# Kernel tuning notes

Measured on AMD Instinct MI355X. Metric: run time of the kernel, lower is better.

## Reference

```python
import jax, jax.numpy as jnp
import numpy as np

HEAD_SIZE = 64


def setup_inputs() -> dict:
    key = jax.random.key(0)
    ks = jax.random.split(key, 6)
    B, S, D, H = 8, 2048, 1024, HEAD_SIZE
    return {
        "q": jax.random.normal(ks[0], (B, S, D), dtype=jnp.float32),
        "k": jax.random.normal(ks[1], (B, S, D), dtype=jnp.float32),
        "v": jax.random.normal(ks[2], (B, S, D), dtype=jnp.float32),
        "mask": jnp.ones((B, S), dtype=bool),
        "Wq": jax.random.normal(ks[3], (D, H), dtype=jnp.float32) * (D ** -0.5),
        "Wk": jax.random.normal(ks[4], (D, H), dtype=jnp.float32) * (D ** -0.5),
        "Wv": jax.random.normal(ks[5], (D, H), dtype=jnp.float32) * (D ** -0.5),
    }


def reference(q, k, v, mask, Wq, Wk, Wv):
    # Linear projections (bias=False): x @ W, W is [n_embd, head_size]
    qp = jnp.einsum("bsd,dh->bsh", q, Wq)
    kp = jnp.einsum("bsd,dh->bsh", k, Wk)
    vp = jnp.einsum("bsd,dh->bsh", v, Wv)
    scale = HEAD_SIZE ** -0.5
    scores = jnp.einsum("bqh,bkh->bqk", qp, kp) * scale  # [B, Sq, Sk]
    # 2-D mask [B, Sk] -> broadcast over query dim (mask.unsqueeze(1))
    scores = jnp.where(mask[:, None, :], scores, -jnp.inf)
    attn = jax.nn.softmax(scores, axis=-1)
    # dropout is identity in eval mode (deterministic reference)
    out = jnp.einsum("bqk,bkh->bqh", attn, vp)
    return out
```

## Files before the change

kernel.cpp:

```cpp
#include <hip/hip_runtime.h>
#include <hip/hip_bf16.h>
#include <math.h>

#define B_ 8
#define S_ 2048
#define D_ 1024
#define H_ 64
#define M_ (B_*S_)
#define SPLIT 4
#define KPS (S_/SPLIT)

typedef __attribute__((ext_vector_type(8))) short bf16x8;
typedef __attribute__((ext_vector_type(8))) unsigned short u16x8;
typedef __attribute__((ext_vector_type(4))) float f32x4;

__device__ inline unsigned short f2bf(float f) {
    unsigned int u = __builtin_bit_cast(unsigned int, f);
    u += 0x7fffu + ((u >> 16) & 1u);
    return (unsigned short)(u >> 16);
}

__device__ inline void async16(const void* g, void* l) {
    __builtin_amdgcn_global_load_lds((const __attribute__((address_space(1))) void*)g,
                                     (__attribute__((address_space(3))) void*)l, 16, 0, 0);
}

__global__ __launch_bounds__(256) void mask_kernel(const unsigned char* __restrict__ mask,
                                                   float* __restrict__ mmul, int n) {
    int j = blockIdx.x * 256 + threadIdx.x;
    if (j >= n) return;
    bool boolLayout = mask[1] != 0;
    int mv = boolLayout ? (int)mask[j] : ((const int*)mask)[j];
    mmul[j] = mv ? 1.0f : 0.0f;
}

__global__ __launch_bounds__(256) void wprep_kernel(
    const float* __restrict__ Wq, const float* __restrict__ Wk, const float* __restrict__ Wv,
    unsigned short* __restrict__ Wt)
{
    const int m = blockIdx.y;
    const float* W = (m == 0) ? Wq : (m == 1) ? Wk : Wv;
    unsigned short* Wo = Wt + (size_t)m * 64 * 1024;
    __shared__ unsigned short T[64][65];
    const int t = threadIdx.x;
    const int k0 = blockIdx.x * 64;
    #pragma unroll
    for (int i = 0; i < 16; i++) {
        int vi = t + i * 256;
        int kk = vi >> 6, n = vi & 63;
        T[kk][n] = f2bf(W[(size_t)(k0 + kk) * 64 + n]);
    }
    __syncthreads();
    #pragma unroll
    for (int i = 0; i < 4; i++) {
        int vi = t + i * 256;
        int n = vi >> 4, k4 = vi & 15;
        ushort4 u;
        u.x = T[k4*4+0][n]; u.y = T[k4*4+1][n]; u.z = T[k4*4+2][n]; u.w = T[k4*4+3][n];
        *(ushort4*)&Wo[(size_t)n * 1024 + k0 + k4*4] = u;
    }
}

__global__ __launch_bounds__(256) void proj_kernel(
    const float* __restrict__ q, const float* __restrict__ kx, const float* __restrict__ vx,
    const unsigned short* __restrict__ Wt,
    unsigned short* __restrict__ qp, unsigned short* __restrict__ kp, unsigned short* __restrict__ vpT)
{
    const int m = blockIdx.y;
    const float* x = (m == 0) ? q : (m == 1) ? kx : vx;
    const unsigned short* Wm = Wt + (size_t)m * 64 * 1024;

    const int t = threadIdx.x;
    const int w = t >> 6, l = t & 63;
    const int lrow = l & 15, quad = l >> 4;
    const int row0 = blockIdx.x * 64;

    const float* xa = x + (size_t)(row0 + w * 16 + lrow) * D_ + quad * 8;
    const unsigned short* wb = Wm + (size_t)lrow * D_ + quad * 8;

    f32x4 acc[4] = {};

    #pragma unroll 2
    for (int k = 0; k < D_; k += 32) {
        f32x4 a0 = *(const f32x4*)(xa + k);
        f32x4 a1 = *(const f32x4*)(xa + k + 4);
        bf16x8 b0 = *(const bf16x8*)(wb + k);
        bf16x8 b1 = *(const bf16x8*)(wb + 16 * D_ + k);
        bf16x8 b2 = *(const bf16x8*)(wb + 32 * D_ + k);
        bf16x8 b3 = *(const bf16x8*)(wb + 48 * D_ + k);
        bf16x8 af;
        af[0] = (short)f2bf(a0.x); af[1] = (short)f2bf(a0.y);
        af[2] = (short)f2bf(a0.z); af[3] = (short)f2bf(a0.w);
        af[4] = (short)f2bf(a1.x); af[5] = (short)f2bf(a1.y);
        af[6] = (short)f2bf(a1.z); af[7] = (short)f2bf(a1.w);
        acc[0] = __builtin_amdgcn_mfma_f32_16x16x32_bf16(af, b0, acc[0], 0, 0, 0);
        acc[1] = __builtin_amdgcn_mfma_f32_16x16x32_bf16(af, b1, acc[1], 0, 0, 0);
        acc[2] = __builtin_amdgcn_mfma_f32_16x16x32_bf16(af, b2, acc[2], 0, 0, 0);
        acc[3] = __builtin_amdgcn_mfma_f32_16x16x32_bf16(af, b3, acc[3], 0, 0, 0);
    }

    const int orow = row0 + w * 16 + quad * 4;
    if (m < 2) {
        unsigned short* outp = (m == 0) ? qp : kp;
        const float sc = (m == 0) ? 0.125f : 1.0f;
        #pragma unroll
        for (int c = 0; c < 4; c++)
            #pragma unroll
            for (int rr = 0; rr < 4; rr++)
                outp[(size_t)(orow + rr) * H_ + c * 16 + lrow] = f2bf(acc[c][rr] * sc);
    } else {
        const int bb = orow >> 11;
        const int s0 = orow & (S_ - 1);
        #pragma unroll
        for (int c = 0; c < 4; c++) {
            ushort4 u;
            u.x = f2bf(acc[c][0]); u.y = f2bf(acc[c][1]);
            u.z = f2bf(acc[c][2]); u.w = f2bf(acc[c][3]);
            *(ushort4*)&vpT[((size_t)bb * H_ + c * 16 + lrow) * S_ + s0] = u;
        }
    }
}

__global__ __launch_bounds__(256) void attn_kernel(
    const unsigned short* __restrict__ qp, const unsigned short* __restrict__ kp,
    const unsigned short* __restrict__ vpT, const float* __restrict__ mmul,
    float* __restrict__ po, float* __restrict__ pl)
{
    __shared__ unsigned short Qs[64][72];
    __shared__ unsigned short Ps[64][72];
    __shared__ unsigned short Ks[64 * 64];
    __shared__ unsigned short Vt[64 * 64];

    const int t = threadIdx.x;
    const int w = t >> 6, l = t & 63;
    const int lrow = l & 15, quad = l >> 4;
    const int b = blockIdx.y, q0 = blockIdx.x * 64, split = blockIdx.z;
    const int key0 = split * KPS;
    const size_t basebs = (size_t)b * S_;
    const unsigned short* vb = vpT + (size_t)b * H_ * S_;

    #pragma unroll
    for (int i = 0; i < 2; i++) {
        int p = t + i * 256;
        int r = p >> 3, c8 = p & 7;
        u16x8 u = *(const u16x8*)&qp[(basebs + q0 + r) * H_ + c8 * 8];
        *(u16x8*)&Qs[r][c8 * 8] = u;
    }

    float lsum[4] = {0.f, 0.f, 0.f, 0.f};
    f32x4 o[4] = {};

    for (int kt = 0; kt < KPS / 64; kt++) {
        const int k0 = key0 + kt * 64;
        __syncthreads();
        #pragma unroll
        for (int j = 0; j < 2; j++) {
            int p = (w * 2 + j) * 64 + l;
            int r = p >> 3;
            int c8 = (p & 7) ^ (r & 7);
            async16(&kp[(basebs + k0 + r) * H_ + c8 * 8], &Ks[p * 8]);
        }
        #pragma unroll
        for (int j = 0; j < 2; j++) {
            int p = (w * 2 + j) * 64 + l;
            int h = p >> 3;
            int c8 = (p & 7) ^ (h & 7);
            async16(&vb[(size_t)h * S_ + k0 + c8 * 8], &Vt[p * 8]);
        }
        float mm[4];
        #pragma unroll
        for (int c = 0; c < 4; c++) mm[c] = mmul[basebs + k0 + c*16 + lrow];
        __syncthreads();

        f32x4 s[4] = {};
        #pragma unroll
        for (int kk = 0; kk < 2; kk++) {
            bf16x8 aq = *(const bf16x8*)&Qs[w*16 + lrow][kk*32 + quad*8];
            #pragma unroll
            for (int c = 0; c < 4; c++) {
                const int n = c*16 + lrow;
                bf16x8 bk = *(const bf16x8*)&Ks[(n * 8 + ((kk*4 + quad) ^ (n & 7))) * 8];
                s[c] = __builtin_amdgcn_mfma_f32_16x16x32_bf16(aq, bk, s[c], 0, 0, 0);
            }
        }
        #pragma unroll
        for (int r = 0; r < 4; r++) {
            float p0 = __expf(s[0][r]) * mm[0];
            float p1 = __expf(s[1][r]) * mm[1];
            float p2 = __expf(s[2][r]) * mm[2];
            float p3 = __expf(s[3][r]) * mm[3];
            lsum[r] += (p0 + p1) + (p2 + p3);
            const int pr = w*16 + quad*4 + r;
            Ps[pr][ 0 + lrow] = f2bf(p0);
            Ps[pr][16 + lrow] = f2bf(p1);
            Ps[pr][32 + lrow] = f2bf(p2);
            Ps[pr][48 + lrow] = f2bf(p3);
        }
        #pragma unroll
        for (int kk = 0; kk < 2; kk++) {
            bf16x8 ap = *(const bf16x8*)&Ps[w*16 + lrow][kk*32 + quad*8];
            #pragma unroll
            for (int c = 0; c < 4; c++) {
                const int h = c*16 + lrow;
                bf16x8 bv = *(const bf16x8*)&Vt[(h * 8 + ((kk*4 + quad) ^ (h & 7))) * 8];
                o[c] = __builtin_amdgcn_mfma_f32_16x16x32_bf16(ap, bv, o[c], 0, 0, 0);
            }
        }
    }

    float* pob = po + (size_t)split * M_ * H_;
    float* plb = pl + (size_t)split * M_;
    #pragma unroll
    for (int r = 0; r < 4; r++) {
        #pragma unroll
        for (int d = 1; d < 16; d <<= 1)
            lsum[r] += __shfl_xor(lsum[r], d, 64);
        const size_t row = basebs + q0 + w*16 + quad*4 + r;
        if (lrow == 0) plb[row] = lsum[r];
        #pragma unroll
        for (int c = 0; c < 4; c++)
            pob[row * H_ + c*16 + lrow] = o[c][r];
    }
}

__global__ __launch_bounds__(256) void combine_kernel(
    const float* __restrict__ po, const float* __restrict__ pl, float* __restrict__ out)
{
    const int idx = blockIdx.x * 256 + threadIdx.x;
    const size_t row = idx >> 4;
    const int c4 = (idx & 15) * 4;
    float lt = 0.f;
    #pragma unroll
    for (int s = 0; s < SPLIT; s++) lt += pl[(size_t)s * M_ + row];
    f32x4 acc = {};
    #pragma unroll
    for (int s = 0; s < SPLIT; s++) {
        const f32x4 p = *(const f32x4*)&po[((size_t)s * M_ + row) * H_ + c4];
        acc += p;
    }
    const float inv = 1.0f / lt;
    f32x4 r = acc * inv;
    *(f32x4*)&out[row * H_ + c4] = r;
}

extern "C" void kernel_launch(void* const* d_in, const int* in_sizes, int n_in,
                              void* d_out, int out_size, void* d_ws, size_t ws_size,
                              hipStream_t stream) {
    const float* q  = (const float*)d_in[0];
    const float* k  = (const float*)d_in[1];
    const float* v  = (const float*)d_in[2];
    const unsigned char* mask = (const unsigned char*)d_in[3];
    const float* Wq = (const float*)d_in[4];
    const float* Wk = (const float*)d_in[5];
    const float* Wv = (const float*)d_in[6];
    float* out = (float*)d_out;

    unsigned short* qp  = (unsigned short*)d_ws;
    unsigned short* kp  = qp + (size_t)M_ * H_;
    unsigned short* vpT = kp + (size_t)M_ * H_;
    float* mmul = (float*)(vpT + (size_t)M_ * H_);
    unsigned short* Wt = (unsigned short*)(mmul + M_);
    float* po = (float*)(Wt + (size_t)3 * 64 * 1024);
    float* pl = po + (size_t)SPLIT * M_ * H_;

    wprep_kernel<<<dim3(16, 3), dim3(256), 0, stream>>>(Wq, Wk, Wv, Wt);
    mask_kernel<<<dim3((M_ + 255)/256), dim3(256), 0, stream>>>(mask, mmul, M_);
    proj_kernel<<<dim3(M_/64, 3), dim3(256), 0, stream>>>(q, k, v, Wt, qp, kp, vpT);
    attn_kernel<<<dim3(S_/64, B_, SPLIT), dim3(256), 0, stream>>>(qp, kp, vpT, mmul, po, pl);
    combine_kernel<<<dim3(M_*16/256), dim3(256), 0, stream>>>(po, pl, out);
}
```

Baseline: 250.7 us.

## Pipeline projection GEMM with async LDS-staged weights and prefetched activations

The projection kernel now stages weight tiles into a 4-deep LDS ring buffer via async global-to-LDS loads with an XOR swizzle. Activation loads are prefetched several k-steps ahead in registers, with manual vmcnt waits and barriers. This is meant to hide global memory latency and share weight loads across the four waves instead of each wave loading from global. It adds barriers every k-step and depends on hand-counted vmcnt values being correct.

```diff
diff --git a/kernel.cpp b/kernel.cpp
--- a/kernel.cpp
+++ b/kernel.cpp
@@ -66,6 +66,8 @@
     const unsigned short* __restrict__ Wt,
     unsigned short* __restrict__ qp, unsigned short* __restrict__ kp, unsigned short* __restrict__ vpT)
 {
+    __shared__ unsigned short Bb[4][64 * 32];
+
     const int m = blockIdx.y;
     const float* x = (m == 0) ? q : (m == 1) ? kx : vx;
     const unsigned short* Wm = Wt + (size_t)m * 64 * 1024;
@@ -76,28 +78,80 @@
     const int row0 = blockIdx.x * 64;
 
     const float* xa = x + (size_t)(row0 + w * 16 + lrow) * D_ + quad * 8;
-    const unsigned short* wb = Wm + (size_t)lrow * D_ + quad * 8;
+
+    const int bn = t >> 2, bu = t & 3;
+    const unsigned short* wsrc = Wm + (size_t)bn * 1024 + (bu ^ (bn & 3)) * 8;
+
+    const int runit = (quad ^ (lrow & 3)) * 8;
 
     f32x4 acc[4] = {};
-
-    #pragma unroll 2
-    for (int k = 0; k < D_; k += 32) {
-        f32x4 a0 = *(const f32x4*)(xa + k);
-        f32x4 a1 = *(const f32x4*)(xa + k + 4);
-        bf16x8 b0 = *(const bf16x8*)(wb + k);
-        bf16x8 b1 = *(const bf16x8*)(wb + 16 * D_ + k);
-        bf16x8 b2 = *(const bf16x8*)(wb + 32 * D_ + k);
-        bf16x8 b3 = *(const bf16x8*)(wb + 48 * D_ + k);
-        bf16x8 af;
-        af[0] = (short)f2bf(a0.x); af[1] = (short)f2bf(a0.y);
-        af[2] = (short)f2bf(a0.z); af[3] = (short)f2bf(a0.w);
-        af[4] = (short)f2bf(a1.x); af[5] = (short)f2bf(a1.y);
-        af[6] = (short)f2bf(a1.z); af[7] = (short)f2bf(a1.w);
-        acc[0] = __builtin_amdgcn_mfma_f32_16x16x32_bf16(af, b0, acc[0], 0, 0, 0);
-        acc[1] = __builtin_amdgcn_mfma_f32_16x16x32_bf16(af, b1, acc[1], 0, 0, 0);
-        acc[2] = __builtin_amdgcn_mfma_f32_16x16x32_bf16(af, b2, acc[2], 0, 0, 0);
-        acc[3] = __builtin_amdgcn_mfma_f32_16x16x32_bf16(af, b3, acc[3], 0, 0, 0);
-    }
+    f32x4 pa0[4], pa1[4];
+
+#define ISSUE_B(kc, buf) do { \
+    async16(wsrc + (kc) * 32, &Bb[buf][t * 8]); \
+    asm volatile("" ::: "memory"); } while (0)
+
+#define LOAD_A(st, kc) do { \
+    pa0[st] = *(const f32x4*)(xa + (kc) * 32); \
+    pa1[st] = *(const f32x4*)(xa + (kc) * 32 + 4); \
+    asm volatile("" ::: "memory"); } while (0)
+
+#define COMPUTE(st, buf) do { \
+    f32x4 a0_ = pa0[st], a1_ = pa1[st]; \
+    bf16x8 af_; \
+    af_[0] = (short)f2bf(a0_.x); af_[1] = (short)f2bf(a0_.y); \
+    af_[2] = (short)f2bf(a0_.z); af_[3] = (short)f2bf(a0_.w); \
+    af_[4] = (short)f2bf(a1_.x); af_[5] = (short)f2bf(a1_.y); \
+    af_[6] = (short)f2bf(a1_.z); af_[7] = (short)f2bf(a1_.w); \
+    bf16x8 b0_ = *(const bf16x8*)&Bb[buf][0 * 512 + lrow * 32 + runit]; \
+    bf16x8 b1_ = *(const bf16x8*)&Bb[buf][1 * 512 + lrow * 32 + runit]; \
+    bf16x8 b2_ = *(const bf16x8*)&Bb[buf][2 * 512 + lrow * 32 + runit]; \
+    bf16x8 b3_ = *(const bf16x8*)&Bb[buf][3 * 512 + lrow * 32 + runit]; \
+    acc[0] = __builtin_amdgcn_mfma_f32_16x16x32_bf16(af_, b0_, acc[0], 0, 0, 0); \
+    acc[1] = __builtin_amdgcn_mfma_f32_16x16x32_bf16(af_, b1_, acc[1], 0, 0, 0); \
+    acc[2] = __builtin_amdgcn_mfma_f32_16x16x32_bf16(af_, b2_, acc[2], 0, 0, 0); \
+    acc[3] = __builtin_amdgcn_mfma_f32_16x16x32_bf16(af_, b3_, acc[3], 0, 0, 0); } while (0)
+
+    ISSUE_B(0, 0); LOAD_A(0, 0);
+    ISSUE_B(1, 1); LOAD_A(1, 1);
+    ISSUE_B(2, 2); LOAD_A(2, 2);
+    LOAD_A(3, 3);
+
+    asm volatile("s_waitcnt vmcnt(0)\n\ts_barrier" ::: "memory");
+    ISSUE_B(3, 3);
+    COMPUTE(0, 0);
+    LOAD_A(0, 4);
+
+    #pragma unroll 1
+    for (int ob = 0; ob < 6; ++ob) {
+        const int kb = ob * 4 + 1;
+        #pragma unroll
+        for (int kk = 0; kk < 4; ++kk) {
+            const int kc = kb + kk;
+            const int st = (kk + 1) & 3;
+            asm volatile("s_waitcnt vmcnt(8)\n\ts_barrier" ::: "memory");
+            ISSUE_B(kc + 3, (st + 3) & 3);
+            COMPUTE(st, st);
+            LOAD_A(st, kc + 4);
+        }
+    }
+    asm volatile("s_waitcnt vmcnt(8)\n\ts_barrier" ::: "memory");
+    ISSUE_B(28, 0); COMPUTE(1, 1); LOAD_A(1, 29);
+    asm volatile("s_waitcnt vmcnt(8)\n\ts_barrier" ::: "memory");
+    ISSUE_B(29, 1); COMPUTE(2, 2); LOAD_A(2, 30);
+    asm volatile("s_waitcnt vmcnt(8)\n\ts_barrier" ::: "memory");
+    ISSUE_B(30, 2); COMPUTE(3, 3); LOAD_A(3, 31);
+    asm volatile("s_waitcnt vmcnt(8)\n\ts_barrier" ::: "memory");
+    ISSUE_B(31, 3);
+    COMPUTE(0, 0);
+    asm volatile("s_waitcnt vmcnt(0)\n\ts_barrier" ::: "memory");
+    COMPUTE(1, 1);
+    COMPUTE(2, 2);
+    COMPUTE(3, 3);
+
+#undef ISSUE_B
+#undef LOAD_A
+#undef COMPUTE
 
     const int orow = row0 + w * 16 + quad * 4;
     if (m < 2) {
```

Result: faster. 243.2 us (-3.0%).

## Stage projection weights in LDS with async double-buffered pipeline

Applied to the files above, without the earlier changes.

The projection kernel's weight operand is now staged cooperatively into a double-buffered LDS tile via async global-to-LDS loads, rather than each wave reading it directly from global memory. Activation loads are software-pipelined several chunks ahead, with hand-placed waitcnt and barrier instructions. This aims to cut redundant global weight traffic and hide load latency behind MFMA work. In exchange it uses 32KB of LDS per block, which may lower occupancy, and relies on fragile manual vmcnt accounting.

```diff
diff --git a/kernel.cpp b/kernel.cpp
--- a/kernel.cpp
+++ b/kernel.cpp
@@ -66,6 +66,8 @@
     const unsigned short* __restrict__ Wt,
     unsigned short* __restrict__ qp, unsigned short* __restrict__ kp, unsigned short* __restrict__ vpT)
 {
+    __shared__ unsigned short Bb[2][4 * 2048];
+
     const int m = blockIdx.y;
     const float* x = (m == 0) ? q : (m == 1) ? kx : vx;
     const unsigned short* Wm = Wt + (size_t)m * 64 * 1024;
@@ -76,28 +78,89 @@
     const int row0 = blockIdx.x * 64;
 
     const float* xa = x + (size_t)(row0 + w * 16 + lrow) * D_ + quad * 8;
-    const unsigned short* wb = Wm + (size_t)lrow * D_ + quad * 8;
+    const unsigned short* wsrc = Wm + (size_t)l * 1024 + w * 8;
+    const int rbase = quad * 512 + lrow * 8;
 
     f32x4 acc[4] = {};
-
-    #pragma unroll 2
-    for (int k = 0; k < D_; k += 32) {
-        f32x4 a0 = *(const f32x4*)(xa + k);
-        f32x4 a1 = *(const f32x4*)(xa + k + 4);
-        bf16x8 b0 = *(const bf16x8*)(wb + k);
-        bf16x8 b1 = *(const bf16x8*)(wb + 16 * D_ + k);
-        bf16x8 b2 = *(const bf16x8*)(wb + 32 * D_ + k);
-        bf16x8 b3 = *(const bf16x8*)(wb + 48 * D_ + k);
-        bf16x8 af;
-        af[0] = (short)f2bf(a0.x); af[1] = (short)f2bf(a0.y);
-        af[2] = (short)f2bf(a0.z); af[3] = (short)f2bf(a0.w);
-        af[4] = (short)f2bf(a1.x); af[5] = (short)f2bf(a1.y);
-        af[6] = (short)f2bf(a1.z); af[7] = (short)f2bf(a1.w);
-        acc[0] = __builtin_amdgcn_mfma_f32_16x16x32_bf16(af, b0, acc[0], 0, 0, 0);
-        acc[1] = __builtin_amdgcn_mfma_f32_16x16x32_bf16(af, b1, acc[1], 0, 0, 0);
-        acc[2] = __builtin_amdgcn_mfma_f32_16x16x32_bf16(af, b2, acc[2], 0, 0, 0);
-        acc[3] = __builtin_amdgcn_mfma_f32_16x16x32_bf16(af, b3, acc[3], 0, 0, 0);
-    }
+    f32x4 pa0[4], pa1[4];
+
+#define STAGE_B(s, buf) do { \
+    _Pragma("unroll") \
+    for (int ch_ = 0; ch_ < 4; ch_++) \
+        async16(wsrc + (s) * 128 + ch_ * 32, &Bb[buf][ch_ * 2048 + t * 8]); \
+    asm volatile("" ::: "memory"); } while (0)
+
+#define LOAD_A(st, ptr) do { \
+    pa0[st] = *(const f32x4*)(ptr); \
+    pa1[st] = *(const f32x4*)((ptr) + 4); \
+    asm volatile("" ::: "memory"); } while (0)
+
+#define COMPUTE(st, ch, base) do { \
+    f32x4 a0_ = pa0[st], a1_ = pa1[st]; \
+    bf16x8 af_; \
+    af_[0] = (short)f2bf(a0_.x); af_[1] = (short)f2bf(a0_.y); \
+    af_[2] = (short)f2bf(a0_.z); af_[3] = (short)f2bf(a0_.w); \
+    af_[4] = (short)f2bf(a1_.x); af_[5] = (short)f2bf(a1_.y); \
+    af_[6] = (short)f2bf(a1_.z); af_[7] = (short)f2bf(a1_.w); \
+    const unsigned short* bp_ = (base) + (ch) * 2048 + rbase; \
+    bf16x8 b0_ = *(const bf16x8*)(bp_); \
+    bf16x8 b1_ = *(const bf16x8*)(bp_ + 128); \
+    bf16x8 b2_ = *(const bf16x8*)(bp_ + 256); \
+    bf16x8 b3_ = *(const bf16x8*)(bp_ + 384); \
+    acc[0] = __builtin_amdgcn_mfma_f32_16x16x32_bf16(af_, b0_, acc[0], 0, 0, 0); \
+    acc[1] = __builtin_amdgcn_mfma_f32_16x16x32_bf16(af_, b1_, acc[1], 0, 0, 0); \
+    acc[2] = __builtin_amdgcn_mfma_f32_16x16x32_bf16(af_, b2_, acc[2], 0, 0, 0); \
+    acc[3] = __builtin_amdgcn_mfma_f32_16x16x32_bf16(af_, b3_, acc[3], 0, 0, 0); } while (0)
+
+    STAGE_B(0, 0);
+    LOAD_A(0, xa + 0);
+    LOAD_A(1, xa + 32);
+    LOAD_A(2, xa + 64);
+    LOAD_A(3, xa + 96);
+    STAGE_B(1, 1);
+
+    asm volatile("s_waitcnt vmcnt(4)\n\ts_barrier" ::: "memory");
+    {
+        const unsigned short* base = &Bb[0][0];
+        const float* xk = xa + 128;
+        COMPUTE(0, 0, base); LOAD_A(0, xk + 0);
+        COMPUTE(1, 1, base); LOAD_A(1, xk + 32);
+        COMPUTE(2, 2, base); LOAD_A(2, xk + 64);
+        COMPUTE(3, 3, base); LOAD_A(3, xk + 96);
+    }
+
+    #pragma unroll 1
+    for (int s = 1; s <= 6; ++s) {
+        const unsigned short* base = &Bb[s & 1][0];
+        const float* xk = xa + (s + 1) * 128;
+        asm volatile("s_waitcnt vmcnt(8)\n\ts_barrier" ::: "memory");
+        STAGE_B(s + 1, (s + 1) & 1);
+        asm volatile("s_waitcnt vmcnt(10)" ::: "memory");
+        COMPUTE(0, 0, base); LOAD_A(0, xk + 0);
+        asm volatile("s_waitcnt vmcnt(10)" ::: "memory");
+        COMPUTE(1, 1, base); LOAD_A(1, xk + 32);
+        asm volatile("s_waitcnt vmcnt(10)" ::: "memory");
+        COMPUTE(2, 2, base); LOAD_A(2, xk + 64);
+        asm volatile("s_waitcnt vmcnt(10)" ::: "memory");
+        COMPUTE(3, 3, base); LOAD_A(3, xk + 96);
+    }
+
+    asm volatile("s_waitcnt vmcnt(8)\n\ts_barrier" ::: "memory");
+    {
+        const unsigned short* base = &Bb[1][0];
+        asm volatile("s_waitcnt vmcnt(6)" ::: "memory");
+        COMPUTE(0, 0, base);
+        asm volatile("s_waitcnt vmcnt(4)" ::: "memory");
+        COMPUTE(1, 1, base);
+        asm volatile("s_waitcnt vmcnt(2)" ::: "memory");
+        COMPUTE(2, 2, base);
+        asm volatile("s_waitcnt vmcnt(0)" ::: "memory");
+        COMPUTE(3, 3, base);
+    }
+
+#undef STAGE_B
+#undef LOAD_A
+#undef COMPUTE
 
     const int orow = row0 + w * 16 + quad * 4;
     if (m < 2) {
```

After: 249.0 us. No clear change (-0.7%).

## Stage projection GEMM tiles through LDS with triple-buffered async loads

Applied to the files above, without the earlier changes.

The projection kernel previously loaded A rows and W columns straight from global memory into registers for every k step. It now streams 64x64 tiles of both operands into a three-deep LDS ring with global_load_lds and uses XOR swizzling to avoid bank conflicts. Each iteration waits on vmcnt and a barrier before computing on the oldest buffer, so loads overlap with MFMA work. This uses about 72KB of LDS per block, which may limit occupancy, and it relies on a hand-written vmcnt count being correct.

```diff
diff --git a/kernel.cpp b/kernel.cpp
--- a/kernel.cpp
+++ b/kernel.cpp
@@ -66,6 +66,9 @@
     const unsigned short* __restrict__ Wt,
     unsigned short* __restrict__ qp, unsigned short* __restrict__ kp, unsigned short* __restrict__ vpT)
 {
+    __shared__ float          As[3][64 * 64];
+    __shared__ unsigned short Bs[3][64 * 64];
+
     const int m = blockIdx.y;
     const float* x = (m == 0) ? q : (m == 1) ? kx : vx;
     const unsigned short* Wm = Wt + (size_t)m * 64 * 1024;
@@ -74,30 +77,68 @@
     const int w = t >> 6, l = t & 63;
     const int lrow = l & 15, quad = l >> 4;
     const int row0 = blockIdx.x * 64;
-
-    const float* xa = x + (size_t)(row0 + w * 16 + lrow) * D_ + quad * 8;
-    const unsigned short* wb = Wm + (size_t)lrow * D_ + quad * 8;
+    const int arow = w * 16 + lrow;
 
     f32x4 acc[4] = {};
 
-    #pragma unroll 2
-    for (int k = 0; k < D_; k += 32) {
-        f32x4 a0 = *(const f32x4*)(xa + k);
-        f32x4 a1 = *(const f32x4*)(xa + k + 4);
-        bf16x8 b0 = *(const bf16x8*)(wb + k);
-        bf16x8 b1 = *(const bf16x8*)(wb + 16 * D_ + k);
-        bf16x8 b2 = *(const bf16x8*)(wb + 32 * D_ + k);
-        bf16x8 b3 = *(const bf16x8*)(wb + 48 * D_ + k);
-        bf16x8 af;
-        af[0] = (short)f2bf(a0.x); af[1] = (short)f2bf(a0.y);
-        af[2] = (short)f2bf(a0.z); af[3] = (short)f2bf(a0.w);
-        af[4] = (short)f2bf(a1.x); af[5] = (short)f2bf(a1.y);
-        af[6] = (short)f2bf(a1.z); af[7] = (short)f2bf(a1.w);
-        acc[0] = __builtin_amdgcn_mfma_f32_16x16x32_bf16(af, b0, acc[0], 0, 0, 0);
-        acc[1] = __builtin_amdgcn_mfma_f32_16x16x32_bf16(af, b1, acc[1], 0, 0, 0);
-        acc[2] = __builtin_amdgcn_mfma_f32_16x16x32_bf16(af, b2, acc[2], 0, 0, 0);
-        acc[3] = __builtin_amdgcn_mfma_f32_16x16x32_bf16(af, b3, acc[3], 0, 0, 0);
-    }
+#define STAGE(s, Ad, Bd) do { \
+    _Pragma("unroll") \
+    for (int j_ = 0; j_ < 4; j_++) {         \
+        int p_ = j_ * 256 + t; \
+        int r_ = p_ >> 4, u_ = p_ & 15; \
+        async16(x + (size_t)(row0 + r_) * D_ + (s) * 64 + ((u_ ^ (r_ & 15)) << 2), \
+                (Ad) + p_ * 4); \
+    } \
+    _Pragma("unroll") \
+    for (int j_ = 0; j_ < 2; j_++) {         \
+        int p_ = j_ * 256 + t; \
+        int n_ = p_ >> 3, ku_ = p_ & 7; \
+        async16(Wm + (size_t)n_ * 1024 + (s) * 64 + ((ku_ ^ (n_ & 7)) << 3), \
+                (Bd) + p_ * 8); \
+    } \
+    asm volatile("" ::: "memory"); } while (0)
+
+#define COMPUTE(Aa, Ba) do { \
+    _Pragma("unroll") \
+    for (int kk_ = 0; kk_ < 2; kk_++) { \
+        const int su_ = kk_ * 8 + quad * 2; \
+        f32x4 a0_ = *(const f32x4*)&(Aa)[arow * 64 + (((su_    ) ^ lrow) << 2)]; \
+        f32x4 a1_ = *(const f32x4*)&(Aa)[arow * 64 + (((su_ + 1) ^ lrow) << 2)]; \
+        bf16x8 af_; \
+        af_[0] = (short)f2bf(a0_.x); af_[1] = (short)f2bf(a0_.y); \
+        af_[2] = (short)f2bf(a0_.z); af_[3] = (short)f2bf(a0_.w); \
+        af_[4] = (short)f2bf(a1_.x); af_[5] = (short)f2bf(a1_.y); \
+        af_[6] = (short)f2bf(a1_.z); af_[7] = (short)f2bf(a1_.w); \
+        _Pragma("unroll") \
+        for (int c_ = 0; c_ < 4; c_++) { \
+            const int n_ = c_ * 16 + lrow; \
+            const int sb_ = (kk_ * 4 + quad) ^ (lrow & 7); \
+            bf16x8 b_ = *(const bf16x8*)&(Ba)[n_ * 64 + sb_ * 8]; \
+            acc[c_] = __builtin_amdgcn_mfma_f32_16x16x32_bf16(af_, b_, acc[c_], 0, 0, 0); \
+        } \
+    } } while (0)
+
+    float *Aa = &As[0][0], *Ab = &As[1][0], *Ac = &As[2][0];
+    unsigned short *Ba = &Bs[0][0], *Bb2 = &Bs[1][0], *Bc = &Bs[2][0];
+
+    STAGE(0, Aa, Ba);
+    STAGE(1, Ab, Bb2);
+
+    #pragma unroll 1
+    for (int s = 0; s < 14; ++s) {
+        asm volatile("s_waitcnt vmcnt(6)\n\ts_barrier" ::: "memory");
+        STAGE(s + 2, Ac, Bc);
+        COMPUTE(Aa, Ba);
+        float* ta = Aa; Aa = Ab; Ab = Ac; Ac = ta;
+        unsigned short* tb = Ba; Ba = Bb2; Bb2 = Bc; Bc = tb;
+    }
+    asm volatile("s_waitcnt vmcnt(6)\n\ts_barrier" ::: "memory");
+    COMPUTE(Aa, Ba);
+    asm volatile("s_waitcnt vmcnt(0)\n\ts_barrier" ::: "memory");
+    COMPUTE(Ab, Bb2);
+
+#undef STAGE
+#undef COMPUTE
 
     const int orow = row0 + w * 16 + quad * 4;
     if (m < 2) {
```

Result: no change. 247.6 us (-1.2%).
